# Kernel optimization log

Hardware: AMD Instinct MI355X
Metric: run time of the kernel (lower is better)

Reference implementation:

```python
import jax, jax.numpy as jnp
import numpy as np


def setup_inputs() -> dict:
    key = jax.random.key(0)
    k1, k2 = jax.random.split(key)
    B, S, D = 8, 2048, 1024
    x = jax.random.normal(k1, (B, S, D), dtype=jnp.float32)
    # xavier_uniform init for [D, D]
    limit = float(np.sqrt(6.0 / (D + D)))
    att_weight = jax.random.uniform(k2, (D, D), dtype=jnp.float32, minval=-limit, maxval=limit)
    bias = jnp.zeros((D,), dtype=jnp.float32)
    return {"x": x, "att_weight": att_weight, "bias": bias}


def reference(x, att_weight, bias):
    # Q = x @ W; K = V = x
    q = jnp.einsum("bsd,de->bse", x, att_weight)
    scale = 1.0 / jnp.sqrt(jnp.asarray(x.shape[-1], dtype=jnp.float32))
    scores = jnp.einsum("bqd,bkd->bqk", q, x) * scale  # [B,S,S]
    attn = jax.nn.softmax(scores, axis=-1)
    out = jnp.einsum("bqk,bkd->bqd", attn, x)
    return out + bias[None, None, :]
```

## Files before the change

### kernel.cpp

```cpp
#include <hip/hip_runtime.h>

typedef unsigned short u16;
typedef unsigned int u32;
typedef __attribute__((ext_vector_type(8))) short short8;
typedef __attribute__((ext_vector_type(4))) float floatx4;

__device__ __forceinline__ u16 f2bf(float f) {
  u32 u = __float_as_uint(f);
  u32 r = u + 0x7fffu + ((u >> 16) & 1u);
  return (u16)(r >> 16);
}

__device__ __forceinline__ void gload_lds16(const u16* g, u16* l) {
  __builtin_amdgcn_global_load_lds(
      (const __attribute__((address_space(1))) u32*)g,
      (__attribute__((address_space(3))) u32*)l, 16, 0, 0);
}

__global__ __launch_bounds__(256)
void cast_tr(const float* __restrict__ in, u16* __restrict__ cast_out,
             u16* __restrict__ tr_out, int rows, int cols, float scale,
             long bstride)
{
  __shared__ u16 tileT[64][66];
  const int b = blockIdx.z;
  in += (long)b * bstride;
  if (cast_out) cast_out += (long)b * bstride;
  tr_out += (long)b * bstride;
  const int r0 = blockIdx.y * 64, c0 = blockIdx.x * 64;
  const int tid = threadIdx.x;

  {
    const int i0 = tid >> 4;
    const int c4 = (tid & 15) * 4;
    #pragma unroll
    for (int rr = 0; rr < 4; ++rr) {
      const int r = i0 + 16 * rr;
      const float4 v = *(const float4*)&in[(long)(r0 + r) * cols + c0 + c4];
      ushort4 h;
      h.x = f2bf(v.x * scale); h.y = f2bf(v.y * scale);
      h.z = f2bf(v.z * scale); h.w = f2bf(v.w * scale);
      if (cast_out)
        *(ushort4*)&cast_out[(long)(r0 + r) * cols + c0 + c4] = h;
      tileT[c4 + 0][r] = h.x;
      tileT[c4 + 1][r] = h.y;
      tileT[c4 + 2][r] = h.z;
      tileT[c4 + 3][r] = h.w;
    }
  }
  __syncthreads();

  {
    const int cb = tid >> 5;
    const int rh = tid & 31;
    #pragma unroll
    for (int m = 0; m < 8; ++m) {
      const int c = cb * 8 + m;
      const u32 pair = *(const u32*)&tileT[c][rh * 2];
      *(u32*)&tr_out[(long)(c0 + c) * rows + r0 + rh * 2] = pair;
    }
  }
}

#define BK 64

template<int MODE, int MI, int NJ>
__global__ __launch_bounds__(256, 3)
void gemm_nt(const u16* __restrict__ A, const u16* __restrict__ Bt,
             void* __restrict__ Cout, const float* __restrict__ bias,
             float* __restrict__ rsum,
             int M, int N, int K, int lda, int ldb, int ldc,
             long sA, long sB, long sC, float escale)
{
  constexpr int BM = MI * 32;
  constexpr int BN = NJ * 32;
  __shared__ __align__(16) u16 As[BM * BK];
  __shared__ __align__(16) u16 Bs[BN * BK];

  const int bz = blockIdx.z;
  A  += (long)bz * sA;
  Bt += (long)bz * sB;

  const int tid  = threadIdx.x;
  const int wave = tid >> 6;
  const int lane = tid & 63;

  const int nbx = gridDim.x, nby = gridDim.y;
  const int pid  = blockIdx.y * nbx + blockIdx.x;
  const int band = 8 * nbx;
  const int gid  = pid / band;
  const int fm   = gid * 8;
  const int gsz  = min(nby - fm, 8);
  const int pm   = fm + (pid % band) % gsz;
  const int pn   = (pid % band) / gsz;
  const int tileM = pm * BM;
  const int tileN = pn * BN;

  const int srow = lane >> 3;
  const int sj   = lane & 7;
  const int sjj  = sj ^ srow;

  const int wm = (wave >> 1) * (MI * 16);
  const int wn = (wave & 1) * (NJ * 16);
  const int lc = lane & 15;
  const int lq = lane >> 4;

  floatx4 acc[MI][NJ];
  #pragma unroll
  for (int i = 0; i < MI; ++i)
    #pragma unroll
    for (int j = 0; j < NJ; ++j)
      acc[i][j] = (floatx4){0.f, 0.f, 0.f, 0.f};

  for (int k0 = 0; k0 < K; k0 += BK) {
    #pragma unroll
    for (int s = 0; s < MI; ++s) {
      const int rb = (wave * MI + s) * 8;
      gload_lds16(A + (long)(tileM + rb + srow) * lda + k0 + sjj * 8,
                  &As[rb * BK]);
    }
    #pragma unroll
    for (int s = 0; s < NJ; ++s) {
      const int rb = (wave * NJ + s) * 8;
      gload_lds16(Bt + (long)(tileN + rb + srow) * ldb + k0 + sjj * 8,
                  &Bs[rb * BK]);
    }
    __syncthreads();

    #pragma unroll
    for (int kk = 0; kk < BK; kk += 32) {
      const int jcb = (kk >> 3) + lq;
      short8 af[MI], bf[NJ];
      #pragma unroll
      for (int i = 0; i < MI; ++i) {
        const int m = wm + i * 16 + lc;
        af[i] = *(const short8*)&As[m * BK + ((jcb ^ (m & 7)) << 3)];
      }
      #pragma unroll
      for (int j = 0; j < NJ; ++j) {
        const int n = wn + j * 16 + lc;
        bf[j] = *(const short8*)&Bs[n * BK + ((jcb ^ (n & 7)) << 3)];
      }
      #pragma unroll
      for (int i = 0; i < MI; ++i)
        #pragma unroll
        for (int j = 0; j < NJ; ++j)
          acc[i][j] = __builtin_amdgcn_mfma_f32_16x16x32_bf16(
                          af[i], bf[j], acc[i][j], 0, 0, 0);
    }
    __syncthreads();
  }

  if (MODE == 0) {
    u16* C = (u16*)Cout + (long)bz * sC;
    #pragma unroll
    for (int i = 0; i < MI; ++i) {
      const int rb = tileM + wm + i * 16 + lq * 4;
      #pragma unroll
      for (int j = 0; j < NJ; ++j) {
        const int col = tileN + wn + j * 16 + lc;
        #pragma unroll
        for (int r = 0; r < 4; ++r)
          C[(long)(rb + r) * ldc + col] = f2bf(acc[i][j][r]);
      }
    }
  } else if (MODE == 1) {
    u16* C = (u16*)Cout + (long)bz * sC;
    float* rs = rsum + (long)bz * M;
    #pragma unroll
    for (int i = 0; i < MI; ++i) {
      const int rb = tileM + wm + i * 16 + lq * 4;
      float rpart[4] = {0.f, 0.f, 0.f, 0.f};
      #pragma unroll
      for (int j = 0; j < NJ; ++j) {
        const int col = tileN + wn + j * 16 + lc;
        #pragma unroll
        for (int r = 0; r < 4; ++r) {
          float e = __expf(acc[i][j][r] * escale);
          C[(long)(rb + r) * ldc + col] = f2bf(e);
          rpart[r] += e;
        }
      }
      #pragma unroll
      for (int r = 0; r < 4; ++r) {
        float s = rpart[r];
        s += __shfl_xor(s, 1, 64);
        s += __shfl_xor(s, 2, 64);
        s += __shfl_xor(s, 4, 64);
        s += __shfl_xor(s, 8, 64);
        if (lc == 0) atomicAdd(&rs[rb + r], s);
      }
    }
  } else {
    float* C = (float*)Cout + (long)bz * sC;
    const float* rs = rsum + (long)bz * M;
    #pragma unroll
    for (int i = 0; i < MI; ++i) {
      const int rb = tileM + wm + i * 16 + lq * 4;
      float inv[4];
      #pragma unroll
      for (int r = 0; r < 4; ++r) inv[r] = 1.0f / rs[rb + r];
      #pragma unroll
      for (int j = 0; j < NJ; ++j) {
        const int col = tileN + wn + j * 16 + lc;
        const float bv = bias[col];
        #pragma unroll
        for (int r = 0; r < 4; ++r)
          C[(long)(rb + r) * ldc + col] = acc[i][j][r] * inv[r] + bv;
      }
    }
  }
}

extern "C" void kernel_launch(void* const* d_in, const int* in_sizes, int n_in,
                              void* d_out, int out_size, void* d_ws, size_t ws_size,
                              hipStream_t stream) {
  const float* x    = (const float*)d_in[0];
  const float* W    = (const float*)d_in[1];
  const float* bias = (const float*)d_in[2];
  float* out        = (float*)d_out;
  (void)in_sizes; (void)n_in; (void)out_size; (void)ws_size;

  const int B = 8, S = 2048, D = 1024;
  const long BSD = (long)B * S * D;

  u16* Xb  = (u16*)d_ws;
  u16* XbT = Xb  + BSD;
  u16* Qb  = XbT + BSD;
  u16* Wt  = Qb  + BSD;
  u16* Sc  = Wt  + (long)D * D;
  float* rsum = (float*)(Sc + (long)B * S * S);

  dim3 blk(256);

  hipMemsetAsync(rsum, 0, (size_t)B * S * sizeof(float), stream);

  cast_tr<<<dim3(D/64, S/64, B), blk, 0, stream>>>(x, Xb, XbT, S, D, 1.0f, (long)S*D);
  cast_tr<<<dim3(D/64, D/64, 1), blk, 0, stream>>>(W, nullptr, Wt, D, D, 0.03125f, 0);

  gemm_nt<0, 4, 4><<<dim3(D/128, (B*S)/128, 1), blk, 0, stream>>>(
      Xb, Wt, Qb, nullptr, nullptr, B*S, D, D, D, D, D, 0, 0, 0, 1.0f);

  gemm_nt<1, 4, 4><<<dim3(S/128, S/128, B), blk, 0, stream>>>(
      Qb, Xb, Sc, nullptr, rsum, S, S, D, D, D, S,
      (long)S*D, (long)S*D, (long)S*S, 1.0f);

  gemm_nt<2, 4, 4><<<dim3(D/128, S/128, B), blk, 0, stream>>>(
      Sc, XbT, out, bias, rsum, S, D, S, S, S, D,
      (long)S*S, (long)D*S, (long)S*D, 1.0f);
}
```

Before: 305.1 us.

## Register-prefetch next K tile instead of direct global-to-LDS loads

Replaces the direct global_load_lds transfers with loads into registers that are issued for the next K tile before the current tile's MFMAs run, then written to LDS at the start of the following iteration. This is meant to overlap global memory latency with compute in all three GEMMs. It adds register pressure (8 short8 staging registers) under launch_bounds(256,3) and an extra VGPR-to-LDS write step.

```diff
diff --git a/kernel.cpp b/kernel.cpp
--- a/kernel.cpp
+++ b/kernel.cpp
@@ -9,12 +9,6 @@
   u32 u = __float_as_uint(f);
   u32 r = u + 0x7fffu + ((u >> 16) & 1u);
   return (u16)(r >> 16);
-}
-
-__device__ __forceinline__ void gload_lds16(const u16* g, u16* l) {
-  __builtin_amdgcn_global_load_lds(
-      (const __attribute__((address_space(1))) u32*)g,
-      (__attribute__((address_space(3))) u32*)l, 16, 0, 0);
 }
 
 __global__ __launch_bounds__(256)
@@ -112,20 +106,45 @@
     for (int j = 0; j < NJ; ++j)
       acc[i][j] = (floatx4){0.f, 0.f, 0.f, 0.f};
 
+  short8 stA[MI], stB[NJ];
+  #pragma unroll
+  for (int s = 0; s < MI; ++s) {
+    const int rb = (wave * MI + s) * 8;
+    stA[s] = *(const short8*)(A + (long)(tileM + rb + srow) * lda + sjj * 8);
+  }
+  #pragma unroll
+  for (int s = 0; s < NJ; ++s) {
+    const int rb = (wave * NJ + s) * 8;
+    stB[s] = *(const short8*)(Bt + (long)(tileN + rb + srow) * ldb + sjj * 8);
+  }
+
   for (int k0 = 0; k0 < K; k0 += BK) {
+    __syncthreads();
     #pragma unroll
     for (int s = 0; s < MI; ++s) {
       const int rb = (wave * MI + s) * 8;
-      gload_lds16(A + (long)(tileM + rb + srow) * lda + k0 + sjj * 8,
-                  &As[rb * BK]);
+      *(short8*)&As[(rb + srow) * BK + sj * 8] = stA[s];
     }
     #pragma unroll
     for (int s = 0; s < NJ; ++s) {
       const int rb = (wave * NJ + s) * 8;
-      gload_lds16(Bt + (long)(tileN + rb + srow) * ldb + k0 + sjj * 8,
-                  &Bs[rb * BK]);
+      *(short8*)&Bs[(rb + srow) * BK + sj * 8] = stB[s];
     }
     __syncthreads();
+
+    const int kn = k0 + BK;
+    if (kn < K) {
+      #pragma unroll
+      for (int s = 0; s < MI; ++s) {
+        const int rb = (wave * MI + s) * 8;
+        stA[s] = *(const short8*)(A + (long)(tileM + rb + srow) * lda + kn + sjj * 8);
+      }
+      #pragma unroll
+      for (int s = 0; s < NJ; ++s) {
+        const int rb = (wave * NJ + s) * 8;
+        stB[s] = *(const short8*)(Bt + (long)(tileN + rb + srow) * ldb + kn + sjj * 8);
+      }
+    }
 
     #pragma unroll
     for (int kk = 0; kk < BK; kk += 32) {
@@ -148,7 +167,6 @@
           acc[i][j] = __builtin_amdgcn_mfma_f32_16x16x32_bf16(
                           af[i], bf[j], acc[i][j], 0, 0, 0);
     }
-    __syncthreads();
   }
 
   if (MODE == 0) {
```

Result: slower. 341.8 us (+12.0%).
